# Kernel optimization log

Hardware: AMD Instinct MI355X
Metric: run time of the kernel (lower is better)

## Reference

```python
import jax, jax.numpy as jnp
import numpy as np

B, T, D_MODEL = 2, 1024, 1024
HEAD_DIM = 128
NUM_HEADS = D_MODEL // HEAD_DIM          # 8
EXPAND_V = 1
HEAD_V = HEAD_DIM * EXPAND_V             # 128
KEY_DIM = NUM_HEADS * HEAD_DIM           # 1024
VALUE_DIM = NUM_HEADS * HEAD_V           # 1024
CONV_SIZE = 4
NUM_LEVELS = int(np.log2(T)) + 1         # 11 Fenwick levels
EPS = 1e-5
SCALE = HEAD_DIM ** -0.5


def setup_inputs() -> dict:
    ks = jax.random.split(jax.random.key(0), 20)
    w = lambda i, shp: 0.02 * jax.random.normal(ks[i], shp, jnp.float32)
    return {
        'x': jax.random.normal(ks[0], (B, T, D_MODEL), jnp.float32),
        'cos': jax.random.normal(ks[1], (T, HEAD_DIM), jnp.float32),
        'sin': jax.random.normal(ks[2], (T, HEAD_DIM), jnp.float32),
        'Wq': w(3, (D_MODEL, KEY_DIM)),
        'Wk': w(4, (D_MODEL, KEY_DIM)),
        'Wv': w(5, (D_MODEL, VALUE_DIM)),
        'Wb': w(6, (D_MODEL, NUM_HEADS)),
        'Wa': w(7, (D_MODEL, NUM_HEADS)),
        'Wl': w(8, (D_MODEL, NUM_HEADS * NUM_LEVELS)),
        'Wg': w(9, (D_MODEL, VALUE_DIM)),
        'Wo': w(10, (VALUE_DIM, D_MODEL)),
        'conv_q': 0.2 * jax.random.normal(ks[11], (KEY_DIM, CONV_SIZE), jnp.float32),
        'conv_k': 0.2 * jax.random.normal(ks[12], (KEY_DIM, CONV_SIZE), jnp.float32),
        'conv_v': 0.2 * jax.random.normal(ks[13], (VALUE_DIM, CONV_SIZE), jnp.float32),
        'A_log': jnp.log(jax.random.uniform(ks[14], (NUM_HEADS,), jnp.float32, 1.0, 16.0)),
        'dt_bias': jnp.log(jnp.expm1(jax.random.uniform(ks[15], (NUM_HEADS,), jnp.float32, 0.001, 0.1))),
        'norm_w': jnp.ones((HEAD_V,), jnp.float32),
    }


def _dwconv_silu(x, w):
    # causal depthwise conv1d (ShortConvolution, activation=silu). x:[B,T,C], w:[C,K]
    xp = jnp.pad(x, ((0, 0), (CONV_SIZE - 1, 0), (0, 0)))
    y = jax.lax.conv_general_dilated(xp, w.T[:, None, :], (1,), 'VALID',
                                     dimension_numbers=('NHC', 'HIO', 'NHC'),
                                     feature_group_count=w.shape[0])
    return jax.nn.silu(y)


def _l2norm(x):
    return x * jax.lax.rsqrt(jnp.sum(x * x, -1, keepdims=True) + 1e-6)


def _levels():
    # Fenwick-tree level of token s (0-indexed) in the prefix decomposition at time t:
    # level(t,s) = floor(log2((t+1) XOR s)) for s <= t.
    n = jnp.arange(1, T + 1, dtype=jnp.int32)[:, None]
    s = jnp.arange(T, dtype=jnp.int32)[None, :]
    xval = jnp.maximum(jnp.bitwise_xor(n, s), 1)
    lev = jnp.floor(jnp.log2(xval.astype(jnp.float32))).astype(jnp.int32)
    return jnp.clip(lev, 0, NUM_LEVELS - 1)  # [T,T]


def _forward(x, Wq, Wk, Wv, Wb, Wa, Wl, Wg, Wo, conv_q, conv_k, conv_v, A_log, dt_bias, norm_w):
    # projections + short conv + silu, split heads -> [B,H,T,d]
    q = _dwconv_silu(x @ Wq, conv_q).reshape(B, T, NUM_HEADS, HEAD_DIM).transpose(0, 2, 1, 3)
    k = _dwconv_silu(x @ Wk, conv_k).reshape(B, T, NUM_HEADS, HEAD_DIM).transpose(0, 2, 1, 3)
    v = _dwconv_silu(x @ Wv, conv_v).reshape(B, T, NUM_HEADS, HEAD_V).transpose(0, 2, 1, 3)
    q = _l2norm(q) * SCALE
    k = _l2norm(k)
    beta = jax.nn.sigmoid(x @ Wb).transpose(0, 2, 1)                      # [B,H,T]
    g = -jnp.exp(A_log) * jax.nn.softplus(x @ Wa + dt_bias)              # [B,T,H] log-decay per step
    gc = jnp.cumsum(g.transpose(0, 2, 1), axis=-1)                        # [B,H,T]
    lam = jax.nn.sigmoid(x @ Wl).reshape(B, T, NUM_HEADS, NUM_LEVELS).transpose(0, 2, 1, 3)  # [B,H,T,L]

    idx = jnp.arange(T)
    causal = idx[:, None] >= idx[None, :]
    strict = idx[:, None] > idx[None, :]
    # stable decay matrix D[t,s] = exp(gc_t - gc_s) <= 1 for s <= t
    logD = gc[..., :, None] - gc[..., None, :]
    Dm = jnp.exp(jnp.where(causal, logD, -jnp.inf))                       # [B,H,T,T]

    # WY / UT transform of the gated delta rule:
    #   u_t = beta_t * v_t - beta_t * sum_{s<t} (k_t . k_s) exp(gc_t-gc_s) u_s
    Akk = jnp.einsum('bhtd,bhsd->bhts', k, k) * Dm * strict
    u = jax.scipy.linalg.solve_triangular(beta[..., None] * Akk,
                                          beta[..., None] * v,
                                          lower=True, unit_diagonal=True)  # [B,H,T,dv]

    # log-linear (hierarchical) readout: o_t = sum_s lam_t[level(t,s)] * (q_t.k_s) D[t,s] * u_s
    P = jnp.einsum('bhtd,bhsd->bhts', q, k) * Dm
    M = jnp.take_along_axis(lam, _levels()[None, None], axis=3)           # [B,H,T,T]
    o = jnp.einsum('bhts,bhsd->bhtd', P * M, u).transpose(0, 2, 1, 3)      # [B,T,H,dv]

    # gated RMSNorm output gate, then output projection
    gate = (x @ Wg).reshape(B, T, NUM_HEADS, HEAD_V)
    o = o * jax.lax.rsqrt(jnp.mean(o * o, -1, keepdims=True) + EPS) * norm_w * jax.nn.silu(gate)
    return o.reshape(B, T, VALUE_DIM) @ Wo


def reference(x, cos, sin, Wq, Wk, Wv, Wb, Wa, Wl, Wg, Wo, conv_q, conv_k, conv_v, A_log, dt_bias, norm_w):
    # cos/sin are accepted (block signature) but unused, matching the source module.
    return _forward(x, Wq, Wk, Wv, Wb, Wa, Wl, Wg, Wo, conv_q, conv_k, conv_v, A_log, dt_bias, norm_w)
```

## Files before the change

kernel.cpp:

```cpp
#include <hip/hip_runtime.h>
#include <hip/hip_bf16.h>
#include <math.h>

#define SCALE_Q 0.08838834764831845f

typedef __bf16 bf16x8 __attribute__((ext_vector_type(8)));
typedef float f32x4 __attribute__((ext_vector_type(4)));

static __device__ __forceinline__ float sigm(float x){ return 1.f/(1.f+__expf(-x)); }
static __device__ __forceinline__ ushort f2b(float v){
  __hip_bfloat16 t = __float2bfloat16(v);
  return __builtin_bit_cast(ushort, t);
}
static __device__ __forceinline__ float b2f(ushort u){
  unsigned v = (unsigned)u << 16; return __builtin_bit_cast(float, v);
}

__global__ __launch_bounds__(256) void prep_all(const float* __restrict__ Wq,
    const float* __restrict__ Wk, const float* __restrict__ Wv,
    const float* __restrict__ Wg, const float* __restrict__ Wo,
    const float* __restrict__ X, const float* __restrict__ Wb,
    const float* __restrict__ Wa, const float* __restrict__ Wl,
    ushort* __restrict__ Wt4, ushort* __restrict__ Wot,
    ushort* __restrict__ x16, float* __restrict__ Wsm)
{
  int z = blockIdx.z;
  int tid = threadIdx.x;
  int flat = blockIdx.y * 32 + blockIdx.x;
  if (z < 5) {
    __shared__ float tile[32][36];
    const float* W = (z==0)?Wq:(z==1)?Wk:(z==2)?Wv:(z==3)?Wg:Wo;
    ushort* Wt = (z<4)? (Wt4 + (size_t)z*1048576) : Wot;
    int n0 = blockIdx.x*32, k0 = blockIdx.y*32;
    int r = tid >> 3, c4 = (tid & 7) << 2;
    *(float4*)&tile[r][c4] = *(const float4*)&W[(size_t)(k0 + r)*1024 + n0 + c4];
    __syncthreads();
    ushort4 o;
    o.x = f2b(tile[c4+0][r]); o.y = f2b(tile[c4+1][r]);
    o.z = f2b(tile[c4+2][r]); o.w = f2b(tile[c4+3][r]);
    *(ushort4*)&Wt[(size_t)(n0 + r)*1024 + k0 + c4] = o;
  } else if (z < 7) {
    int idx = (z-5)*262144 + flat*256 + tid;
    float4 v = *(const float4*)&X[(size_t)idx*4];
    ushort4 o; o.x=f2b(v.x); o.y=f2b(v.y); o.z=f2b(v.z); o.w=f2b(v.w);
    *(ushort4*)&x16[(size_t)idx*4] = o;
  } else {
    int idx = flat*256 + tid;
    if (idx < 1024*104) {
      int k = idx / 104, c = idx % 104;
      float v = (c < 8) ? Wb[k*8+c] : (c < 16) ? Wa[k*8+(c-8)] : Wl[k*88+(c-16)];
      Wsm[idx] = v;
    }
  }
}

__global__ __launch_bounds__(256) void gemm_bf16(const ushort* __restrict__ A,
    const ushort* __restrict__ Bt, void* __restrict__ C0, void* __restrict__ C1,
    int M, int N, int K, int nsplit, int ld0, int ld1, int c0bf16, int c1bf16)
{
  __shared__ ushort As[3][128*32];
  __shared__ ushort Bs[3][128*32];
  int tid = threadIdx.x;
  int gx = gridDim.x;
  int nwg = gx * gridDim.y;
  int id = blockIdx.y * gx + blockIdx.x;
  int id2 = (id & 7) * (nwg >> 3) + (id >> 3);
  int bm = (id2 / gx) * 128, bn = (id2 % gx) * 128;
  int wave = tid >> 6, lane = tid & 63;
  int wm = (wave >> 1) * 64, wn = (wave & 1) * 64;
  int l16 = lane & 15, kh = lane >> 4;
  f32x4 acc[4][4] = {};
  int rowA0 = tid >> 2, boA = (tid & 3) * 16;
  int niter = K >> 5;

  #pragma unroll
  for (int s = 0; s < 2; ++s) {
    int k0 = s << 5;
    #pragma unroll
    for (int j = 0; j < 2; ++j) {
      int row = rowA0 + j*64;
      const char* gA = (const char*)A + (((size_t)(bm+row)*K + k0)*2 + boA);
      const char* gB = (const char*)Bt + (((size_t)(bn+row)*K + k0)*2 + boA);
      __builtin_amdgcn_global_load_lds((const __attribute__((address_space(1))) unsigned*)gA,
        (__attribute__((address_space(3))) unsigned*)((char*)&As[s][0] + row*64 + boA), 16, 0, 0);
      __builtin_amdgcn_global_load_lds((const __attribute__((address_space(1))) unsigned*)gB,
        (__attribute__((address_space(3))) unsigned*)((char*)&Bs[s][0] + row*64 + boA), 16, 0, 0);
    }
  }
  asm volatile("s_waitcnt vmcnt(4)" ::: "memory");
  __builtin_amdgcn_s_barrier();
  __builtin_amdgcn_sched_barrier(0);
  for (int i = 0; i < niter; ++i) {
    int cur = i % 3;
    if (i + 2 < niter) {
      int k0 = (i+2) << 5;
      int nb = (i+2) % 3;
      char* al = (char*)&As[nb][0];
      char* bl = (char*)&Bs[nb][0];
      #pragma unroll
      for (int j = 0; j < 2; ++j) {
        int row = rowA0 + j*64;
        const char* gA = (const char*)A + (((size_t)(bm+row)*K + k0)*2 + boA);
        const char* gB = (const char*)Bt + (((size_t)(bn+row)*K + k0)*2 + boA);
        __builtin_amdgcn_global_load_lds((const __attribute__((address_space(1))) unsigned*)gA,
          (__attribute__((address_space(3))) unsigned*)(al + row*64 + boA), 16, 0, 0);
        __builtin_amdgcn_global_load_lds((const __attribute__((address_space(1))) unsigned*)gB,
          (__attribute__((address_space(3))) unsigned*)(bl + row*64 + boA), 16, 0, 0);
      }
    }
    bf16x8 af[4], bfr[4];
    #pragma unroll
    for (int ii = 0; ii < 4; ++ii)
      af[ii] = *(bf16x8*)((char*)&As[cur][0] + (wm + ii*16 + l16)*64 + kh*16);
    #pragma unroll
    for (int j = 0; j < 4; ++j)
      bfr[j] = *(bf16x8*)((char*)&Bs[cur][0] + (wn + j*16 + l16)*64 + kh*16);
    #pragma unroll
    for (int ii = 0; ii < 4; ++ii)
      #pragma unroll
      for (int j = 0; j < 4; ++j)
        acc[ii][j] = __builtin_amdgcn_mfma_f32_16x16x32_bf16(af[ii], bfr[j], acc[ii][j], 0, 0, 0);
    if (i + 1 < niter) {
      if (i + 2 < niter) {
        asm volatile("s_waitcnt vmcnt(4) lgkmcnt(0)" ::: "memory");
      } else {
        asm volatile("s_waitcnt vmcnt(0) lgkmcnt(0)" ::: "memory");
      }
      __builtin_amdgcn_s_barrier();
      __builtin_amdgcn_sched_barrier(0);
    }
  }
  int rg = lane >> 4;
  #pragma unroll
  for (int i = 0; i < 4; ++i) {
    #pragma unroll
    for (int j = 0; j < 4; ++j) {
      int col = bn + wn + j*16 + l16;
      #pragma unroll
      for (int r = 0; r < 4; ++r) {
        int row = bm + wm + i*16 + rg*4 + r;
        float v = acc[i][j][r];
        if (col < nsplit) {
          if (c0bf16) ((ushort*)C0)[(size_t)row*ld0 + col] = f2b(v);
          else        ((float*)C0)[(size_t)row*ld0 + col] = v;
        } else {
          if (c1bf16) ((ushort*)C1)[(size_t)row*ld1 + (col - nsplit)] = f2b(v);
          else        ((float*)C1)[(size_t)row*ld1 + (col - nsplit)] = v;
        }
      }
    }
  }
}

__global__ __launch_bounds__(128) void gemm_wo64(const ushort* __restrict__ A,
    const ushort* __restrict__ Bt, float* __restrict__ C, int K)
{
  __shared__ ushort As[3][64*32];
  __shared__ ushort Bs[3][128*32];
  int tid = threadIdx.x;
  int gx = gridDim.x;
  int nwg = gx * gridDim.y;
  int id = blockIdx.y * gx + blockIdx.x;
  int id2 = (id & 7) * (nwg >> 3) + (id >> 3);
  int bm = (id2 / gx) * 64, bn = (id2 % gx) * 128;
  int wave = tid >> 6, lane = tid & 63;
  int wn = wave * 64;
  int l16 = lane & 15, kh = lane >> 4;
  f32x4 acc[4][4] = {};
  int rowA0 = tid >> 2, boA = (tid & 3) * 16;
  int niter = K >> 5;

  #pragma unroll
  for (int s = 0; s < 2; ++s) {
    int k0 = s << 5;
    #pragma unroll
    for (int j = 0; j < 2; ++j) {
      int row = rowA0 + j*32;
      const char* gA = (const char*)A + (((size_t)(bm+row)*K + k0)*2 + boA);
      __builtin_amdgcn_global_load_lds((const __attribute__((address_space(1))) unsigned*)gA,
        (__attribute__((address_space(3))) unsigned*)((char*)&As[s][0] + row*64 + boA), 16, 0, 0);
    }
    #pragma unroll
    for (int j = 0; j < 4; ++j) {
      int row = rowA0 + j*32;
      const char* gB = (const char*)Bt + (((size_t)(bn+row)*K + k0)*2 + boA);
      __builtin_amdgcn_global_load_lds((const __attribute__((address_space(1))) unsigned*)gB,
        (__attribute__((address_space(3))) unsigned*)((char*)&Bs[s][0] + row*64 + boA), 16, 0, 0);
    }
  }
  asm volatile("s_waitcnt vmcnt(6)" ::: "memory");
  __builtin_amdgcn_s_barrier();
  __builtin_amdgcn_sched_barrier(0);
  for (int i = 0; i < niter; ++i) {
    int cur = i % 3;
    if (i + 2 < niter) {
      int k0 = (i+2) << 5;
      int nb = (i+2) % 3;
      char* al = (char*)&As[nb][0];
      char* bl = (char*)&Bs[nb][0];
      #pragma unroll
      for (int j = 0; j < 2; ++j) {
        int row = rowA0 + j*32;
        const char* gA = (const char*)A + (((size_t)(bm+row)*K + k0)*2 + boA);
        __builtin_amdgcn_global_load_lds((const __attribute__((address_space(1))) unsigned*)gA,
          (__attribute__((address_space(3))) unsigned*)(al + row*64 + boA), 16, 0, 0);
      }
      #pragma unroll
      for (int j = 0; j < 4; ++j) {
        int row = rowA0 + j*32;
        const char* gB = (const char*)Bt + (((size_t)(bn+row)*K + k0)*2 + boA);
        __builtin_amdgcn_global_load_lds((const __attribute__((address_space(1))) unsigned*)(gB),
          (__attribute__((address_space(3))) unsigned*)(bl + row*64 + boA), 16, 0, 0);
      }
    }
    bf16x8 af[4], bfr[4];
    #pragma unroll
    for (int ii = 0; ii < 4; ++ii)
      af[ii] = *(bf16x8*)((char*)&As[cur][0] + (ii*16 + l16)*64 + kh*16);
    #pragma unroll
    for (int j = 0; j < 4; ++j)
      bfr[j] = *(bf16x8*)((char*)&Bs[cur][0] + (wn + j*16 + l16)*64 + kh*16);
    #pragma unroll
    for (int ii = 0; ii < 4; ++ii)
      #pragma unroll
      for (int j = 0; j < 4; ++j)
        acc[ii][j] = __builtin_amdgcn_mfma_f32_16x16x32_bf16(af[ii], bfr[j], acc[ii][j], 0, 0, 0);
    if (i + 1 < niter) {
      if (i + 2 < niter) {
        asm volatile("s_waitcnt vmcnt(6) lgkmcnt(0)" ::: "memory");
      } else {
        asm volatile("s_waitcnt vmcnt(0) lgkmcnt(0)" ::: "memory");
      }
      __builtin_amdgcn_s_barrier();
      __builtin_amdgcn_sched_barrier(0);
    }
  }
  int rg = lane >> 4;
  #pragma unroll
  for (int i = 0; i < 4; ++i) {
    #pragma unroll
    for (int j = 0; j < 4; ++j) {
      int col = bn + wn + j*16 + l16;
      #pragma unroll
      for (int r = 0; r < 4; ++r) {
        int row = bm + i*16 + rg*4 + r;
        C[(size_t)row*1024 + col] = acc[i][j][r];
      }
    }
  }
}

__global__ __launch_bounds__(256) void skinny104(const float* __restrict__ X,
    const float* __restrict__ Wsm, float* __restrict__ part)
{
  __shared__ float XL[64][132];
  __shared__ float WsL[128][112];
  int tid = threadIdx.x;
  int m0 = blockIdx.x << 6;
  int k0 = blockIdx.y << 7;
  #pragma unroll
  for (int j = 0; j < 8; ++j) {
    int s = tid + j*256;
    int row = s >> 5, c4 = (s & 31) << 2;
    *(float4*)&XL[row][c4] = *(const float4*)&X[(size_t)(m0 + row)*1024 + k0 + c4];
  }
  {
    int k = tid >> 1, c = 104 + ((tid & 1) << 2);
    *(float4*)&WsL[k][c] = (float4){0.f,0.f,0.f,0.f};
  }
  {
    int k = tid >> 1, cb = (tid & 1) * 52;
    #pragma unroll
    for (int j = 0; j < 13; ++j) {
      *(float4*)&WsL[k][cb + j*4] = *(const float4*)&Wsm[(size_t)(k0 + k)*104 + cb + j*4];
    }
  }
  __syncthreads();
  int row = tid >> 2, cq = tid & 3;
  int cbase = cq * 28;
  f32x4 acc[7] = {};
  const float* xrow = &XL[row][0];
  #pragma unroll 4
  for (int k = 0; k < 128; ++k) {
    float xv = xrow[k];
    const f32x4* wr = (const f32x4*)&WsL[k][cbase];
    #pragma unroll
    for (int j = 0; j < 7; ++j) acc[j] += xv * wr[j];
  }
  float* pr = &part[((size_t)blockIdx.y*2048 + m0 + row)*104 + cbase];
  int nst = (cq == 3) ? 5 : 7;
  for (int j = 0; j < nst; ++j) *(f32x4*)&pr[j*4] = acc[j];
}

__global__ __launch_bounds__(256) void reduce8(const float* __restrict__ part,
    float* __restrict__ xs)
{
  int idx = blockIdx.x*256 + threadIdx.x;
  if (idx >= 212992) return;
  float s = 0.f;
  #pragma unroll
  for (int i = 0; i < 8; ++i) s += part[(size_t)i*212992 + idx];
  xs[idx] = s;
}

__global__ __launch_bounds__(256) void conv_fused(const ushort* __restrict__ Xall,
    const float* __restrict__ Wq, const float* __restrict__ Wk, const float* __restrict__ Wv,
    ushort* __restrict__ qb16, ushort* __restrict__ kb16, ushort* __restrict__ vb16, int ldx)
{
  int mode = blockIdx.y;
  const float* W = (mode==0)?Wq:(mode==1)?Wk:Wv;
  const ushort* X = Xall + mode*1024;
  int row = blockIdx.x;
  int b = row >> 10, t = row & 1023;
  int tid = threadIdx.x;
  int c0 = tid << 2;
  float w[4][4];
  #pragma unroll
  for (int c = 0; c < 4; ++c) {
    float4 wv = *(const float4*)&W[(c0 + c)*4];
    w[c][0]=wv.x; w[c][1]=wv.y; w[c][2]=wv.z; w[c][3]=wv.w;
  }
  float acc[4] = {0.f,0.f,0.f,0.f};
  #pragma unroll
  for (int j = 0; j < 4; ++j) {
    int tt = t - 3 + j;
    if (tt >= 0) {
      ushort4 xv = *(const ushort4*)&X[(size_t)(b*1024 + tt)*ldx + c0];
      acc[0] += w[0][j]*b2f(xv.x); acc[1] += w[1][j]*b2f(xv.y);
      acc[2] += w[2][j]*b2f(xv.z); acc[3] += w[3][j]*b2f(xv.w);
    }
  }
  #pragma unroll
  for (int c = 0; c < 4; ++c) acc[c] *= sigm(acc[c]);
  if (mode < 2) {
    float ss = acc[0]*acc[0]+acc[1]*acc[1]+acc[2]*acc[2]+acc[3]*acc[3];
    ss += __shfl_xor(ss, 1); ss += __shfl_xor(ss, 2); ss += __shfl_xor(ss, 4);
    ss += __shfl_xor(ss, 8); ss += __shfl_xor(ss, 16);
    float r = rsqrtf(ss + 1e-6f);
    if (mode == 0) r *= SCALE_Q;
    acc[0]*=r; acc[1]*=r; acc[2]*=r; acc[3]*=r;
  }
  size_t o = (size_t)(b*1024 + t)*1024 + c0;
  ushort* Y = (mode==0)?qb16:(mode==1)?kb16:vb16;
  ushort4 yb; yb.x=f2b(acc[0]); yb.y=f2b(acc[1]); yb.z=f2b(acc[2]); yb.w=f2b(acc[3]);
  *(ushort4*)&Y[o] = yb;
}

__global__ __launch_bounds__(256) void gc2(const float* __restrict__ xs,
    const float* __restrict__ A_log, const float* __restrict__ dt_bias,
    float* __restrict__ gc)
{
  int bh = blockIdx.x, b = bh >> 3, h = bh & 7;
  __shared__ float sc[256];
  int tid = threadIdx.x;
  float aexp = __expf(A_log[h]), db = dt_bias[h];
  int t0 = tid*4;
  float g[4], csum = 0.f;
  #pragma unroll
  for (int z = 0; z < 4; ++z) {
    float zv = xs[(size_t)(b*1024 + t0 + z)*104 + 8 + h] + db;
    float sp = (zv > 20.f) ? zv : log1pf(__expf(zv));
    csum += -aexp*sp;
    g[z] = csum;
  }
  sc[tid] = csum;
  __syncthreads();
  for (int ofs = 1; ofs < 256; ofs <<= 1) {
    float v = (tid >= ofs) ? sc[tid-ofs] : 0.f;
    __syncthreads();
    sc[tid] += v;
    __syncthreads();
  }
  float excl = sc[tid] - csum;
  #pragma unroll
  for (int z = 0; z < 4; ++z) gc[bh*1024 + t0 + z] = excl + g[z];
}

__global__ __launch_bounds__(256) void chunk_prep(const ushort* __restrict__ Kg16,
    const ushort* __restrict__ Vg16, const float* __restrict__ xs,
    const float* __restrict__ gcg, float* __restrict__ cw, ushort* __restrict__ cWk16,
    ushort* __restrict__ cKpT16, float* __restrict__ eD)
{
  int blk = blockIdx.x;
  int bh = blk >> 4, ck = blk & 15;
  int b = bh >> 3, h = bh & 7;
  int a = ck << 6;
  __shared__ ushort Kl[64*128];
  __shared__ float As[64][68];
  __shared__ float gcl[65];
  __shared__ float bl[64];
  __shared__ float egc[64];
  __shared__ float edt[64];
  int tid = threadIdx.x;
  int wave = tid >> 6, lane = tid & 63;
  int l15 = lane & 15, kh = lane >> 4;
  for (int e = tid; e < 2048; e += 256) {
    int t = e >> 5;
    int c4u = (e & 31) << 2;
    ushort4 kv = *(const ushort4*)&Kg16[(size_t)(b*1024 + a + t)*1024 + h*128 + c4u];
    unsigned slot = (unsigned)(c4u >> 3) ^ (unsigned)(t & 15);
    *(ushort4*)((char*)Kl + t*256 + slot*16 + (c4u & 7)*2) = kv;
  }
  if (tid < 64) {
    gcl[tid] = gcg[bh*1024 + a + tid];
    bl[tid] = sigm(xs[(size_t)(b*1024 + a + tid)*104 + h]);
  }
  if (tid == 64) gcl[64] = (ck < 15) ? gcg[bh*1024 + a + 64] : 0.f;
  __syncthreads();
  if (tid < 64) {
    egc[tid] = __expf(gcl[tid] - gcl[0]);
    edt[tid] = (ck < 15) ? __expf(gcl[64] - gcl[tid]) : 0.f;
  }
  {
    int arow = wave*16 + l15;
    int asw = arow & 15;
    for (int jt = 0; jt <= wave; ++jt) {
      int brow = jt*16 + l15;
      int bsw = brow & 15;
      f32x4 acc = {0.f,0.f,0.f,0.f};
      #pragma unroll
      for (int ks = 0; ks < 4; ++ks) {
        bf16x8 afr = *(const bf16x8*)((char*)Kl + arow*256 + (((ks*4 + kh) ^ asw) << 4));
        bf16x8 bfr = *(const bf16x8*)((char*)Kl + brow*256 + (((ks*4 + kh) ^ bsw) << 4));
        acc = __builtin_amdgcn_mfma_f32_16x16x32_bf16(afr, bfr, acc, 0, 0, 0);
      }
      int s = jt*16 + l15;
      #pragma unroll
      for (int r = 0; r < 4; ++r) {
        int t = wave*16 + kh*4 + r;
        if (s < t) As[t][s] = bl[t]*acc[r]*__expf(gcl[t]-gcl[s]);
      }
    }
  }
  __syncthreads();
  int c = tid;
  float u[64];
  if (c < 128) {
    #pragma unroll
    for (int t = 0; t < 64; ++t)
      u[t] = bl[t]*b2f(Vg16[(size_t)(b*1024 + a + t)*1024 + h*128 + c]);
  } else {
    int d = c - 128;
    unsigned dslot = (unsigned)(d >> 3);
    #pragma unroll
    for (int t = 0; t < 64; ++t) {
      ushort kv = *(const ushort*)((char*)Kl + t*256 + ((dslot ^ (unsigned)(t & 15)) << 4) + (d & 7)*2);
      u[t] = bl[t]*egc[t]*b2f(kv);
    }
  }
  #pragma unroll
  for (int t = 1; t < 64; ++t) {
    float acc = u[t];
    int s = 0;
    #pragma unroll
    for (; s + 4 <= t; s += 4) {
      float4 a4 = *(float4*)&As[t][s];
      acc -= a4.x*u[s] + a4.y*u[s+1] + a4.z*u[s+2] + a4.w*u[s+3];
    }
    #pragma unroll
    for (; s < t; ++s) acc -= As[t][s]*u[s];
    u[t] = acc;
  }
  size_t cbase = (size_t)blk*8192;
  if (c < 128) {
    #pragma unroll
    for (int t = 0; t < 64; ++t)
      cw[cbase + t*128 + c] = u[t];
  } else {
    int d = c - 128;
    unsigned dslot = (unsigned)(d >> 3);
    #pragma unroll
    for (int t = 0; t < 64; ++t) {
      cWk16[cbase + t*128 + d] = f2b(-u[t]);
      ushort kv = *(const ushort*)((char*)Kl + t*256 + ((dslot ^ (unsigned)(t & 15)) << 4) + (d & 7)*2);
      cKpT16[cbase + d*64 + t] = f2b(b2f(kv)*edt[t]);
    }
  }
  if (tid == 0) eD[blk] = (ck < 15) ? __expf(gcl[64]-gcl[0]) : 0.f;
}

__global__ __launch_bounds__(256) void chunk_scan6(const float* __restrict__ cw,
    const ushort* __restrict__ cWk16, const ushort* __restrict__ cKpT16,
    const float* __restrict__ eD, ushort* __restrict__ Ut)
{
  int blk = blockIdx.x;
  int slice = blk >> 4, bh = blk & 15;
  int e_base = slice << 3;
  __shared__ ushort Wks[2][8192];
  __shared__ ushort Kps[2][8192];
  __shared__ ushort StT[16*128];
  __shared__ ushort usT[16*64];
  __shared__ float  Stf[128*16];
  int tid = threadIdx.x;
  int wave = tid >> 6, lane = tid & 63;
  int l15 = lane & 15, kh = lane >> 4;
  for (int idx = tid; idx < 16*128; idx += 256) StT[idx] = 0;
  for (int idx = tid; idx < 16*64; idx += 256) usT[idx] = 0;
  for (int idx = tid; idx < 128*16; idx += 256) Stf[idx] = 0.f;

  int e = l15;
  int t0 = wave*16 + kh*4;
  int ci0 = bh << 4;
  f32x4 wcur = {0.f,0.f,0.f,0.f};
  if (e < 8) {
    #pragma unroll
    for (int r = 0; r < 4; ++r)
      wcur[r] = cw[(size_t)ci0*8192 + (t0+r)*128 + e_base + e];
  }
  {
    const char* wg = (const char*)(cWk16 + (size_t)ci0*8192);
    const char* kg = (const char*)(cKpT16 + (size_t)ci0*8192);
    #pragma unroll
    for (int j = 0; j < 4; ++j) {
      unsigned off = (j<<12) + (tid<<4);
      unsigned wrow = off >> 8, wslot = (off >> 4) & 15;
      unsigned wsrc = wrow*256 + ((wslot ^ (wrow & 15)) << 4);
      __builtin_amdgcn_global_load_lds((const __attribute__((address_space(1))) unsigned*)(wg + wsrc),
        (__attribute__((address_space(3))) unsigned*)((char*)&Wks[0][0] + off), 16, 0, 0);
      unsigned krow = off >> 7, kslot = (off >> 4) & 7;
      unsigned ksrc = krow*128 + ((kslot ^ (krow & 7)) << 4);
      __builtin_amdgcn_global_load_lds((const __attribute__((address_space(1))) unsigned*)(kg + ksrc),
        (__attribute__((address_space(3))) unsigned*)((char*)&Kps[0][0] + off), 16, 0, 0);
    }
  }
  __syncthreads();

  for (int i = 0; i < 16; ++i) {
    int ci = ci0 + i, a = i << 6, cur = i & 1;
    f32x4 wnext = {0.f,0.f,0.f,0.f};
    if (i < 15) {
      if (e < 8) {
        #pragma unroll
        for (int r = 0; r < 4; ++r)
          wnext[r] = cw[(size_t)(ci+1)*8192 + (t0+r)*128 + e_base + e];
      }
      const char* wg = (const char*)(cWk16 + (size_t)(ci+1)*8192);
      const char* kg = (const char*)(cKpT16 + (size_t)(ci+1)*8192);
      char* wl = (char*)&Wks[cur^1][0];
      char* kl = (char*)&Kps[cur^1][0];
      #pragma unroll
      for (int j = 0; j < 4; ++j) {
        unsigned off = (j<<12) + (tid<<4);
        unsigned wrow = off >> 8, wslot = (off >> 4) & 15;
        unsigned wsrc = wrow*256 + ((wslot ^ (wrow & 15)) << 4);
        __builtin_amdgcn_global_load_lds((const __attribute__((address_space(1))) unsigned*)(wg + wsrc),
          (__attribute__((address_space(3))) unsigned*)(wl + off), 16, 0, 0);
        unsigned krow = off >> 7, kslot = (off >> 4) & 7;
        unsigned ksrc = krow*128 + ((kslot ^ (krow & 7)) << 4);
        __builtin_amdgcn_global_load_lds((const __attribute__((address_space(1))) unsigned*)(kg + ksrc),
          (__attribute__((address_space(3))) unsigned*)(kl + off), 16, 0, 0);
      }
    }
    {
      f32x4 d = wcur;
      const char* wkb = (const char*)&Wks[cur][0];
      int arow = wave*16 + l15;
      #pragma unroll
      for (int ks = 0; ks < 4; ++ks) {
        bf16x8 afr = *(const bf16x8*)(wkb + arow*256 + (((ks*4 + kh) ^ l15) << 4));
        bf16x8 bfr = *(const bf16x8*)((const char*)StT + l15*256 + (((ks*4 + kh) ^ l15) << 4));
        d = __builtin_amdgcn_mfma_f32_16x16x32_bf16(afr, bfr, d, 0, 0, 0);
      }
      if (e < 8) {
        ushort4 uw;
        uw.x = f2b(d[0]); uw.y = f2b(d[1]); uw.z = f2b(d[2]); uw.w = f2b(d[3]);
        *(ushort4*)((char*)usT + e*128 + (((t0>>3) ^ (e&7)) << 4) + (t0&7)*2) = uw;
        *(ushort4*)&Ut[(size_t)(bh*128 + e_base + e)*1024 + a + t0] = uw;
      }
    }
    asm volatile("s_waitcnt lgkmcnt(0)" ::: "memory");
    __builtin_amdgcn_s_barrier();
    __builtin_amdgcn_sched_barrier(0);
    if (i < 15) {
      float ed = eD[ci];
      const char* kpb = (const char*)&Kps[cur][0];
      #pragma unroll
      for (int mt = 0; mt < 2; ++mt) {
        int krow = (wave*2 + mt)*16 + l15;
        int k0 = (wave*2 + mt)*16 + kh*4;
        f32x4 c;
        #pragma unroll
        for (int r = 0; r < 4; ++r) c[r] = ed * Stf[(k0+r)*16 + e];
        #pragma unroll
        for (int ts = 0; ts < 2; ++ts) {
          bf16x8 afr = *(const bf16x8*)(kpb + krow*128 + (((ts*4 + kh) ^ (krow&7)) << 4));
          bf16x8 bfr = *(const bf16x8*)((const char*)usT + l15*128 + (((ts*4 + kh) ^ (l15&7)) << 4));
          c = __builtin_amdgcn_mfma_f32_16x16x32_bf16(afr, bfr, c, 0, 0, 0);
        }
        #pragma unroll
        for (int r = 0; r < 4; ++r) Stf[(k0+r)*16 + e] = c[r];
        if (e < 8) {
          ushort4 sw;
          sw.x = f2b(c[0]); sw.y = f2b(c[1]); sw.z = f2b(c[2]); sw.w = f2b(c[3]);
          *(ushort4*)((char*)StT + e*256 + (((k0>>3) ^ e) << 4) + (k0&7)*2) = sw;
        }
      }
      wcur = wnext;
      asm volatile("s_waitcnt vmcnt(0) lgkmcnt(0)" ::: "memory");
      __builtin_amdgcn_s_barrier();
      __builtin_amdgcn_sched_barrier(0);
    }
  }
}

__global__ __launch_bounds__(256) void readout3(const ushort* __restrict__ Qb,
    const ushort* __restrict__ Kb, const ushort* __restrict__ Ut,
    const float* __restrict__ gcg, const float* __restrict__ xs,
    float* __restrict__ Og)
{
  int blk = blockIdx.x;
  int bh = blk >> 4, ic = blk & 15;
  int half = blockIdx.y;
  int b = bh >> 3, h = bh & 7;
  int tbase = ic << 6;
  __shared__ ushort Ks[2][8192];
  __shared__ ushort Us[2][8192];
  __shared__ ushort Pl[4][1024];
  __shared__ float lamS[64][12];
  int tid = threadIdx.x;
  int wave = tid >> 6, lane = tid & 63;
  int l15 = lane & 15, kh = lane >> 4;

  const char* kgb = (const char*)Kb + ((size_t)(b*1024)*1024 + h*128)*2;
  const char* ugb = (const char*)Ut + ((size_t)(bh*128)*1024)*2;

  for (int e = tid; e < 64*11; e += 256) {
    int t = e/11, l = e%11;
    lamS[t][l] = sigm(xs[(size_t)(b*1024+tbase+t)*104 + 16 + h*11 + l]);
  }
  int tl = kh*4;
  float gct_r[4];
  #pragma unroll
  for (int r = 0; r < 4; ++r) gct_r[r] = gcg[bh*1024 + tbase + wave*16 + tl + r];
  bf16x8 qf[4];
  {
    const ushort* qp = &Qb[(size_t)(b*1024 + tbase + wave*16 + l15)*1024 + h*128 + kh*8];
    #pragma unroll
    for (int kk = 0; kk < 4; ++kk) qf[kk] = *(const bf16x8*)(qp + kk*32);
  }

  f32x4 accO[8] = {};
  int nsteps = ic + 1;
  int jmid = (nsteps + 1) >> 1;
  int j0 = half ? jmid : 0;
  int j1 = half ? nsteps : jmid;
  ushort* Pw = &Pl[wave][0];

  if (j0 < j1) {
    {
      const char* kg = kgb + (size_t)(j0<<6)*2048;
      const char* ug = ugb + (size_t)(j0<<6)*2;
      #pragma unroll
      for (int it = 0; it < 4; ++it) {
        unsigned off = (it<<12) + (tid<<4);
        unsigned krow = off >> 8, kc = (off >> 4) & 15;
        unsigned ksrc = krow*2048 + ((kc ^ (krow & 15)) << 4);
        __builtin_amdgcn_global_load_lds((const __attribute__((address_space(1))) unsigned*)(kg + ksrc),
          (__attribute__((address_space(3))) unsigned*)((char*)&Ks[0][0] + off), 16, 0, 0);
        unsigned ud = off >> 7, uc = (off >> 4) & 7;
        unsigned usrc = ud*2048 + ((uc ^ (ud & 7)) << 4);
        __builtin_amdgcn_global_load_lds((const __attribute__((address_space(1))) unsigned*)(ug + usrc),
          (__attribute__((address_space(3))) unsigned*)((char*)&Us[0][0] + off), 16, 0, 0);
      }
    }
    __syncthreads();
    int cur = 0;
    for (int j = j0; j < j1; ++j) {
      int sbase = j << 6;
      if (j + 1 < j1) {
        const char* kg = kgb + (size_t)((j+1)<<6)*2048;
        const char* ug = ugb + (size_t)((j+1)<<6)*2;
        char* kl = (char*)&Ks[cur^1][0];
        char* ul = (char*)&Us[cur^1][0];
        #pragma unroll
        for (int it = 0; it < 4; ++it) {
          unsigned off = (it<<12) + (tid<<4);
          unsigned krow = off >> 8, kc = (off >> 4) & 15;
          unsigned ksrc = krow*2048 + ((kc ^ (krow & 15)) << 4);
          __builtin_amdgcn_global_load_lds((const __attribute__((address_space(1))) unsigned*)(kg + ksrc),
            (__attribute__((address_space(3))) unsigned*)(kl + off), 16, 0, 0);
          unsigned ud = off >> 7, uc = (off >> 4) & 7;
          unsigned usrc = ud*2048 + ((uc ^ (ud & 7)) << 4);
          __builtin_amdgcn_global_load_lds((const __attribute__((address_space(1))) unsigned*)(ug + usrc),
            (__attribute__((address_space(3))) unsigned*)(ul + off), 16, 0, 0);
        }
      }
      float gcs_r[4];
      #pragma unroll
      for (int jt = 0; jt < 4; ++jt)
        gcs_r[jt] = gcg[bh*1024 + sbase + jt*16 + l15];
      f32x4 accS[4] = {};
      const char* ksb = (const char*)&Ks[cur][0];
      #pragma unroll
      for (int jt = 0; jt < 4; ++jt) {
        int row = jt*16 + l15;
        int rsw = row & 15;
        #pragma unroll
        for (int kk = 0; kk < 4; ++kk) {
          bf16x8 kf = *(const bf16x8*)(ksb + row*256 + (((kk*4 + kh) ^ rsw) << 4));
          accS[jt] = __builtin_amdgcn_mfma_f32_16x16x32_bf16(qf[kk], kf, accS[jt], 0, 0, 0);
        }
      }
      #pragma unroll
      for (int jt = 0; jt < 4; ++jt) {
        int sg = sbase + jt*16 + l15;
        #pragma unroll
        for (int r = 0; r < 4; ++r) {
          int t_loc = tl + r;
          int tg = tbase + wave*16 + t_loc;
          float pv = 0.f;
          if (sg <= tg) {
            int lev = 31 - __clz((unsigned)((tg+1) ^ sg));
            lev = lev > 10 ? 10 : lev;
            pv = accS[jt][r] * __expf(gct_r[r] - gcs_r[jt]) * lamS[wave*16 + t_loc][lev];
          }
          int bo = (t_loc << 7) + ((jt*16 + l15) << 1);
          bo ^= (t_loc & 7) << 4;
          *(ushort*)((char*)Pw + bo) = f2b(pv);
        }
      }
      const char* usb = (const char*)&Us[cur][0];
      #pragma unroll
      for (int ks = 0; ks < 2; ++ks) {
        int bo = (l15 << 7) + ((ks*32 + kh*8) << 1);
        bo ^= (l15 & 7) << 4;
        bf16x8 pa = *(bf16x8*)((char*)Pw + bo);
        #pragma unroll
        for (int dt = 0; dt < 8; ++dt) {
          int d = dt*16 + l15;
          bf16x8 uf = *(const bf16x8*)(usb + d*128 + (((ks*4 + kh) ^ (d & 7)) << 4));
          accO[dt] = __builtin_amdgcn_mfma_f32_16x16x32_bf16(pa, uf, accO[dt], 0, 0, 0);
        }
      }
      __syncthreads();
      cur ^= 1;
    }
  }
  float* og = Og + (size_t)half*2097152;
  #pragma unroll
  for (int dt = 0; dt < 8; ++dt) {
    #pragma unroll
    for (int r = 0; r < 4; ++r) {
      int row = tbase + wave*16 + tl + r;
      og[(size_t)(b*1024 + row)*1024 + h*128 + dt*16 + l15] = accO[dt][r];
    }
  }
}

__global__ __launch_bounds__(256) void normgate(const float* __restrict__ O1,
    const float* __restrict__ O2, const ushort* __restrict__ G16,
    const float* __restrict__ norm_w, ushort* __restrict__ Y)
{
  int row = blockIdx.x*4 + (threadIdx.x >> 6);
  int lane = threadIdx.x & 63;
  size_t base = (size_t)(row >> 3)*1024 + (size_t)(row & 7)*128;
  float2 oa = *(const float2*)&O1[base + lane*2];
  float2 ob = *(const float2*)&O2[base + lane*2];
  float ox = oa.x + ob.x, oy = oa.y + ob.y;
  float ss = ox*ox + oy*oy;
  #pragma unroll
  for (int m = 1; m < 64; m <<= 1) ss += __shfl_xor(ss, m);
  float r = rsqrtf(ss * (1.f/128.f) + 1e-5f);
  ushort2 g16 = *(const ushort2*)&G16[base + lane*2];
  float gx = b2f(g16.x), gy = b2f(g16.y);
  ushort2 y;
  y.x = f2b(ox * r * norm_w[lane*2+0] * (gx * sigm(gx)));
  y.y = f2b(oy * r * norm_w[lane*2+1] * (gy * sigm(gy)));
  *(ushort2*)&Y[base + lane*2] = y;
}

extern "C" void kernel_launch(void* const* d_in, const int* in_sizes, int n_in,
                              void* d_out, int out_size, void* d_ws, size_t ws_size,
                              hipStream_t stream)
{
  const float* x    = (const float*)d_in[0];
  const float* Wq   = (const float*)d_in[3];
  const float* Wk   = (const float*)d_in[4];
  const float* Wv   = (const float*)d_in[5];
  const float* Wb   = (const float*)d_in[6];
  const float* Wa   = (const float*)d_in[7];
  const float* Wl   = (const float*)d_in[8];
  const float* Wg   = (const float*)d_in[9];
  const float* Wo   = (const float*)d_in[10];
  const float* cq   = (const float*)d_in[11];
  const float* ck   = (const float*)d_in[12];
  const float* cv   = (const float*)d_in[13];
  const float* A_log   = (const float*)d_in[14];
  const float* dt_bias = (const float*)d_in[15];
  const float* norm_w  = (const float*)d_in[16];
  float* out = (float*)d_out;

  float* p = (float*)d_ws;
  float* xqkv = p;  p += 6291456;
  float* xg   = p;  p += 2097152;
  float* kbu  = p;  p += 2097152;
  float* vbu  = p;  p += 2097152;
  float* o1   = p;  p += 2097152;
  float* o2   = p;  p += 2097152;
  float* xs   = p;  p += 212992;
  float* gc   = p;  p += 16384;
  float* eD   = p;  p += 256;
  ushort* x16 = (ushort*)p; p += 1048576;
  ushort* Wt4 = (ushort*)p; p += 2097152;
  ushort* Wot = (ushort*)p; p += 524288;
  float* Wsm  = p;  p += 106496;
  ushort* yb16= (ushort*)p; p += 1048576;
  ushort* qb16= (ushort*)p; p += 1048576;
  ushort* kb16= (ushort*)p; p += 1048576;
  ushort* ut16= (ushort*)p; p += 1048576;
  ushort* xqkv16 = (ushort*)xqkv;
  ushort* xg16 = (ushort*)xg;
  ushort* vb16 = (ushort*)vbu;
  float* cw  = xqkv;
  ushort* cWk16  = (ushort*)(xqkv + 2097152);
  ushort* cKpT16 = (ushort*)(xqkv + 3145728);
  float* part = o1;
  (void)kbu;

  dim3 blk(256);
  prep_all<<<dim3(32,32,8), blk, 0, stream>>>(Wq, Wk, Wv, Wg, Wo, x, Wb, Wa, Wl,
                                              Wt4, Wot, x16, Wsm);
  gemm_bf16<<<dim3(32,16), blk, 0, stream>>>(x16, Wt4, xqkv16, xg16, 2048, 4096, 1024,
                                             3072, 3072, 1024, 1, 1);
  skinny104<<<dim3(32,8), blk, 0, stream>>>(x, Wsm, part);
  reduce8<<<dim3(833), blk, 0, stream>>>(part, xs);
  conv_fused<<<dim3(2048,3), blk, 0, stream>>>(xqkv16, cq, ck, cv, qb16, kb16, vb16, 3072);
  gc2<<<dim3(16), blk, 0, stream>>>(xs, A_log, dt_bias, gc);
  chunk_prep<<<dim3(256), blk, 0, stream>>>(kb16, vb16, xs, gc, cw, cWk16, cKpT16, eD);
  chunk_scan6<<<dim3(256), blk, 0, stream>>>(cw, cWk16, cKpT16, eD, ut16);
  readout3<<<dim3(256,2), blk, 0, stream>>>(qb16, kb16, ut16, gc, xs, o1);
  normgate<<<dim3(4096), blk, 0, stream>>>(o1, o2, xg16, norm_w, yb16);
  gemm_wo64<<<dim3(8,32), dim3(128), 0, stream>>>(yb16, Wot, out, 1024);
}
```

Measured before the change: 189.7 us.

## Fold split-K reduction into consumers and split readout into four key-range quarters

Removes the reduce8 kernel: gc2, chunk_prep and readout3 now sum the eight skinny104 partials on the fly wherever they need the small projection values. Separately, readout3's grid grows from two to four slices of the causal key-chunk range, and normgate sums four partial outputs instead of two. This drops one launch and raises parallelism for the triangular readout. In exchange, partial sums are re-read redundantly and normgate carries extra output traffic.

```diff
diff --git a/kernel.cpp b/kernel.cpp
--- a/kernel.cpp
+++ b/kernel.cpp
@@ -14,6 +14,12 @@
 }
 static __device__ __forceinline__ float b2f(ushort u){
   unsigned v = (unsigned)u << 16; return __builtin_bit_cast(float, v);
+}
+static __device__ __forceinline__ float sum8(const float* __restrict__ p, int idx){
+  float s = 0.f;
+  #pragma unroll
+  for (int i = 0; i < 8; ++i) s += p[(size_t)i*212992 + idx];
+  return s;
 }
 
 __global__ __launch_bounds__(256) void prep_all(const float* __restrict__ Wq,
@@ -292,17 +298,6 @@
   for (int j = 0; j < nst; ++j) *(f32x4*)&pr[j*4] = acc[j];
 }
 
-__global__ __launch_bounds__(256) void reduce8(const float* __restrict__ part,
-    float* __restrict__ xs)
-{
-  int idx = blockIdx.x*256 + threadIdx.x;
-  if (idx >= 212992) return;
-  float s = 0.f;
-  #pragma unroll
-  for (int i = 0; i < 8; ++i) s += part[(size_t)i*212992 + idx];
-  xs[idx] = s;
-}
-
 __global__ __launch_bounds__(256) void conv_fused(const ushort* __restrict__ Xall,
     const float* __restrict__ Wq, const float* __restrict__ Wk, const float* __restrict__ Wv,
     ushort* __restrict__ qb16, ushort* __restrict__ kb16, ushort* __restrict__ vb16, int ldx)
@@ -346,7 +341,7 @@
   *(ushort4*)&Y[o] = yb;
 }
 
-__global__ __launch_bounds__(256) void gc2(const float* __restrict__ xs,
+__global__ __launch_bounds__(256) void gc2(const float* __restrict__ part,
     const float* __restrict__ A_log, const float* __restrict__ dt_bias,
     float* __restrict__ gc)
 {
@@ -358,7 +353,7 @@
   float g[4], csum = 0.f;
   #pragma unroll
   for (int z = 0; z < 4; ++z) {
-    float zv = xs[(size_t)(b*1024 + t0 + z)*104 + 8 + h] + db;
+    float zv = sum8(part, (b*1024 + t0 + z)*104 + 8 + h) + db;
     float sp = (zv > 20.f) ? zv : log1pf(__expf(zv));
     csum += -aexp*sp;
     g[z] = csum;
@@ -377,7 +372,7 @@
 }
 
 __global__ __launch_bounds__(256) void chunk_prep(const ushort* __restrict__ Kg16,
-    const ushort* __restrict__ Vg16, const float* __restrict__ xs,
+    const ushort* __restrict__ Vg16, const float* __restrict__ part,
     const float* __restrict__ gcg, float* __restrict__ cw, ushort* __restrict__ cWk16,
     ushort* __restrict__ cKpT16, float* __restrict__ eD)
 {
@@ -403,7 +398,7 @@
   }
   if (tid < 64) {
     gcl[tid] = gcg[bh*1024 + a + tid];
-    bl[tid] = sigm(xs[(size_t)(b*1024 + a + tid)*104 + h]);
+    bl[tid] = sigm(sum8(part, (b*1024 + a + tid)*104 + h));
   }
   if (tid == 64) gcl[64] = (ck < 15) ? gcg[bh*1024 + a + 64] : 0.f;
   __syncthreads();
@@ -605,12 +600,12 @@
 
 __global__ __launch_bounds__(256) void readout3(const ushort* __restrict__ Qb,
     const ushort* __restrict__ Kb, const ushort* __restrict__ Ut,
-    const float* __restrict__ gcg, const float* __restrict__ xs,
+    const float* __restrict__ gcg, const float* __restrict__ part,
     float* __restrict__ Og)
 {
   int blk = blockIdx.x;
   int bh = blk >> 4, ic = blk & 15;
-  int half = blockIdx.y;
+  int quarter = blockIdx.y;
   int b = bh >> 3, h = bh & 7;
   int tbase = ic << 6;
   __shared__ ushort Ks[2][8192];
@@ -626,7 +621,7 @@
 
   for (int e = tid; e < 64*11; e += 256) {
     int t = e/11, l = e%11;
-    lamS[t][l] = sigm(xs[(size_t)(b*1024+tbase+t)*104 + 16 + h*11 + l]);
+    lamS[t][l] = sigm(sum8(part, (b*1024+tbase+t)*104 + 16 + h*11 + l));
   }
   int tl = kh*4;
   float gct_r[4];
@@ -641,9 +636,8 @@
 
   f32x4 accO[8] = {};
   int nsteps = ic + 1;
-  int jmid = (nsteps + 1) >> 1;
-  int j0 = half ? jmid : 0;
-  int j1 = half ? nsteps : jmid;
+  int j0 = (nsteps * quarter) >> 2;
+  int j1 = (nsteps * (quarter + 1)) >> 2;
   ushort* Pw = &Pl[wave][0];
 
   if (j0 < j1) {
@@ -736,7 +730,7 @@
       cur ^= 1;
     }
   }
-  float* og = Og + (size_t)half*2097152;
+  float* og = Og + (size_t)quarter*2097152;
   #pragma unroll
   for (int dt = 0; dt < 8; ++dt) {
     #pragma unroll
@@ -747,16 +741,19 @@
   }
 }
 
-__global__ __launch_bounds__(256) void normgate(const float* __restrict__ O1,
-    const float* __restrict__ O2, const ushort* __restrict__ G16,
-    const float* __restrict__ norm_w, ushort* __restrict__ Y)
+__global__ __launch_bounds__(256) void normgate(const float* __restrict__ O,
+    const ushort* __restrict__ G16, const float* __restrict__ norm_w,
+    ushort* __restrict__ Y)
 {
   int row = blockIdx.x*4 + (threadIdx.x >> 6);
   int lane = threadIdx.x & 63;
   size_t base = (size_t)(row >> 3)*1024 + (size_t)(row & 7)*128;
-  float2 oa = *(const float2*)&O1[base + lane*2];
-  float2 ob = *(const float2*)&O2[base + lane*2];
-  float ox = oa.x + ob.x, oy = oa.y + ob.y;
+  float ox = 0.f, oy = 0.f;
+  #pragma unroll
+  for (int q = 0; q < 4; ++q) {
+    float2 ov = *(const float2*)&O[(size_t)q*2097152 + base + lane*2];
+    ox += ov.x; oy += ov.y;
+  }
   float ss = ox*ox + oy*oy;
   #pragma unroll
   for (int m = 1; m < 64; m <<= 1) ss += __shfl_xor(ss, m);
@@ -793,11 +790,9 @@
   float* p = (float*)d_ws;
   float* xqkv = p;  p += 6291456;
   float* xg   = p;  p += 2097152;
-  float* kbu  = p;  p += 2097152;
+  float* part = p;  p += 2097152;
   float* vbu  = p;  p += 2097152;
-  float* o1   = p;  p += 2097152;
-  float* o2   = p;  p += 2097152;
-  float* xs   = p;  p += 212992;
+  float* o1   = p;  p += 8388608;
   float* gc   = p;  p += 16384;
   float* eD   = p;  p += 256;
   ushort* x16 = (ushort*)p; p += 1048576;
@@ -814,8 +809,6 @@
   float* cw  = xqkv;
   ushort* cWk16  = (ushort*)(xqkv + 2097152);
   ushort* cKpT16 = (ushort*)(xqkv + 3145728);
-  float* part = o1;
-  (void)kbu;
 
   dim3 blk(256);
   prep_all<<<dim3(32,32,8), blk, 0, stream>>>(Wq, Wk, Wv, Wg, Wo, x, Wb, Wa, Wl,
@@ -823,12 +816,11 @@
   gemm_bf16<<<dim3(32,16), blk, 0, stream>>>(x16, Wt4, xqkv16, xg16, 2048, 4096, 1024,
                                              3072, 3072, 1024, 1, 1);
   skinny104<<<dim3(32,8), blk, 0, stream>>>(x, Wsm, part);
-  reduce8<<<dim3(833), blk, 0, stream>>>(part, xs);
   conv_fused<<<dim3(2048,3), blk, 0, stream>>>(xqkv16, cq, ck, cv, qb16, kb16, vb16, 3072);
-  gc2<<<dim3(16), blk, 0, stream>>>(xs, A_log, dt_bias, gc);
-  chunk_prep<<<dim3(256), blk, 0, stream>>>(kb16, vb16, xs, gc, cw, cWk16, cKpT16, eD);
+  gc2<<<dim3(16), blk, 0, stream>>>(part, A_log, dt_bias, gc);
+  chunk_prep<<<dim3(256), blk, 0, stream>>>(kb16, vb16, part, gc, cw, cWk16, cKpT16, eD);
   chunk_scan6<<<dim3(256), blk, 0, stream>>>(cw, cWk16, cKpT16, eD, ut16);
-  readout3<<<dim3(256,2), blk, 0, stream>>>(qb16, kb16, ut16, gc, xs, o1);
-  normgate<<<dim3(4096), blk, 0, stream>>>(o1, o2, xg16, norm_w, yb16);
+  readout3<<<dim3(256,4), blk, 0, stream>>>(qb16, kb16, ut16, gc, part, o1);
+  normgate<<<dim3(4096), blk, 0, stream>>>(o1, xg16, norm_w, yb16);
   gemm_wo64<<<dim3(8,32), dim3(128), 0, stream>>>(yb16, Wot, out, 1024);
 }
```

Result: slower. 201.1 us (+6.0%).
